# Kernel tuning notes

Measured on AMD Instinct MI355X. Metric: run time of the kernel, lower is better.

## Reference

```python
import jax, jax.numpy as jnp
import numpy as np
import math

B, S, D, H = 2, 2048, 1024, 32
HD = D // H  # head_dim = 32
NEG = -1e9


def setup_inputs() -> dict:
    key = jax.random.key(0)
    ks = jax.random.split(key, 6)
    x = jax.random.normal(ks[0], (B, S, D), dtype=jnp.float32)
    # additive causal mask: 0 on/below diagonal, -1e9 above
    causal = jnp.tril(jnp.ones((S, S), dtype=bool))
    mask = jnp.where(causal, 0.0, NEG).astype(jnp.float32)[None, None]
    # SSMax-style per-query-position log-length scale
    section_log_len = jnp.log(jnp.arange(1, S + 1, dtype=jnp.float32) + 1.0).reshape(1, 1, S, 1)
    sc = 1.0 / math.sqrt(D)
    wq = jax.random.normal(ks[1], (D, D), dtype=jnp.float32) * sc
    wk = jax.random.normal(ks[2], (D, D), dtype=jnp.float32) * sc
    wv = jax.random.normal(ks[3], (D, D), dtype=jnp.float32) * sc
    wo = jax.random.normal(ks[4], (D, D), dtype=jnp.float32) * sc
    seq_scale = jnp.ones((1, H, 1, 1), dtype=jnp.float32)
    return {"x": x, "mask": mask, "section_log_len": section_log_len,
            "wq": wq, "wk": wk, "wv": wv, "wo": wo, "seq_scale": seq_scale}


def reference(x, mask, section_log_len, wq, wk, wv, wo, seq_scale):
    bsz, seqlen, dim = x.shape
    # projections (torch Linear: y = x @ W.T); split heads -> [b, h, s, hd]
    q = (x @ wq.T).reshape(bsz, seqlen, H, HD).transpose(0, 2, 1, 3)
    k = (x @ wk.T).reshape(bsz, seqlen, H, HD).transpose(0, 2, 1, 3)
    v = (x @ wv.T).reshape(bsz, seqlen, H, HD).transpose(0, 2, 1, 3)
    # n_kv_heads == n_heads, so repeat_kv is identity
    scores = jnp.einsum('bhqd,bhkd->bhqk', q, k) / math.sqrt(HD)
    scores = scores * (section_log_len * seq_scale)  # SSMax per-head learned scale
    scores = scores + mask
    probs = jax.nn.softmax(scores.astype(jnp.float32), axis=-1).astype(q.dtype)
    out = jnp.einsum('bhqk,bhkd->bhqd', probs, v)
    out = out.transpose(0, 2, 1, 3).reshape(bsz, seqlen, dim)
    return out @ wo.T
```

## Files before the change

kernel.cpp:

```cpp
#include <hip/hip_runtime.h>
#include <hip/hip_bf16.h>

typedef __bf16 bf16_t;
typedef bf16_t bf16x8 __attribute__((ext_vector_type(8)));
typedef float f32x4 __attribute__((ext_vector_type(4)));

#define NB 2
#define SEQ 2048
#define DIM 1024
#define NH 32
#define HDIM 32

#define LDA 40

static __device__ __forceinline__ f32x4 mfma16(bf16x8 a, bf16x8 b, f32x4 c) {
    return __builtin_amdgcn_mfma_f32_16x16x32_bf16(a, b, c, 0, 0, 0);
}

__global__ __launch_bounds__(256)
void cvt_x(const float* __restrict__ src, bf16_t* __restrict__ dst, int n) {
    const int stride = gridDim.x * blockDim.x;
    const int nv = n >> 2;
    for (int i = blockIdx.x * blockDim.x + threadIdx.x; i < nv; i += stride) {
        float4 v = ((const float4*)src)[i];
        bf16_t o[4] = {(bf16_t)v.x, (bf16_t)v.y, (bf16_t)v.z, (bf16_t)v.w};
        *(uint2*)(dst + i * 4) = *(const uint2*)o;
    }
}

template <int MODE, typename CT>
__global__ __launch_bounds__(256)
void gemm_bt(const bf16_t* __restrict__ A, const float* __restrict__ W,
             CT* __restrict__ C) {
    __shared__ alignas(16) bf16_t As[128 * LDA];
    __shared__ alignas(16) bf16_t Bs[64 * LDA];
    const int t = threadIdx.x;
    const int lane = t & 63;
    const int wave = t >> 6;
    const int lane16 = lane & 15;
    const int quad = lane >> 4;
    const int wm = (wave >> 1) * 64;
    const int wn = (wave & 1) * 32;
    const int m0 = blockIdx.y * 128;
    const int n0 = blockIdx.x * 64;
    const int ar = t >> 2;
    const int ac = (t & 3) * 8;

    f32x4 acc[4][2];
#pragma unroll
    for (int i = 0; i < 4; i++)
#pragma unroll
        for (int j = 0; j < 2; j++) acc[i][j] = f32x4{0.f, 0.f, 0.f, 0.f};

    for (int k0 = 0; k0 < DIM; k0 += 32) {
        uint4 a0 = *(const uint4*)(A + (m0 + ar) * DIM + k0 + ac);
        uint4 a1 = *(const uint4*)(A + (m0 + 64 + ar) * DIM + k0 + ac);
        float4 w0 = *(const float4*)(W + (n0 + ar) * DIM + k0 + ac);
        float4 w1 = *(const float4*)(W + (n0 + ar) * DIM + k0 + ac + 4);
        bf16_t wb[8] = {(bf16_t)w0.x, (bf16_t)w0.y, (bf16_t)w0.z, (bf16_t)w0.w,
                        (bf16_t)w1.x, (bf16_t)w1.y, (bf16_t)w1.z, (bf16_t)w1.w};
        __syncthreads();
        *(uint4*)(As + ar * LDA + ac) = a0;
        *(uint4*)(As + (64 + ar) * LDA + ac) = a1;
        *(uint4*)(Bs + ar * LDA + ac) = *(const uint4*)wb;
        __syncthreads();
        bf16x8 af[4], bfr[2];
#pragma unroll
        for (int mi = 0; mi < 4; mi++)
            af[mi] = *(const bf16x8*)(As + (wm + mi * 16 + lane16) * LDA + quad * 8);
#pragma unroll
        for (int ni = 0; ni < 2; ni++)
            bfr[ni] = *(const bf16x8*)(Bs + (wn + ni * 16 + lane16) * LDA + quad * 8);
#pragma unroll
        for (int mi = 0; mi < 4; mi++)
#pragma unroll
            for (int ni = 0; ni < 2; ni++)
                acc[mi][ni] = (MODE == 2) ? mfma16(bfr[ni], af[mi], acc[mi][ni])
                                          : mfma16(af[mi], bfr[ni], acc[mi][ni]);
    }

#pragma unroll
    for (int mi = 0; mi < 4; mi++)
#pragma unroll
        for (int ni = 0; ni < 2; ni++)
#pragma unroll
            for (int r = 0; r < 4; r++) {
                float v = acc[mi][ni][r];
                if (MODE == 0) {
                    int row = m0 + wm + mi * 16 + quad * 4 + r;
                    int col = n0 + wn + ni * 16 + lane16;
                    C[row * DIM + col] = (CT)v;
                } else if (MODE == 1) {
                    int m = m0 + wm + mi * 16 + quad * 4 + r;
                    int n = n0 + wn + ni * 16 + lane16;
                    int b = m >> 11, s = m & (SEQ - 1);
                    int h = n >> 5, d = n & 31;
                    C[(((b * NH + h) * SEQ + s) << 5) + d] = (CT)v;
                } else {
                    int n = n0 + wn + ni * 16 + quad * 4 + r;
                    int m = m0 + wm + mi * 16 + lane16;
                    int b = m >> 11, s = m & (SEQ - 1);
                    int h = n >> 5, d = n & 31;
                    C[(((b * NH + h) * HDIM + d) << 11) + s] = (CT)v;
                }
            }
}

__global__ __launch_bounds__(256)
void attn_fwd(const bf16_t* __restrict__ q, const bf16_t* __restrict__ k,
              const bf16_t* __restrict__ vt, const float* __restrict__ slen,
              const float* __restrict__ sscale, bf16_t* __restrict__ out) {
    __shared__ alignas(16) bf16_t pscr[4][32 * LDA];
    const int t = threadIdx.x;
    const int lane = t & 63, wave = t >> 6;
    const int lane16 = lane & 15, quad = lane >> 4;
    const int gw = blockIdx.x * 4 + wave;
    const int idx = gw & 63;
    const int qt = (idx & 1) ? (63 - (idx >> 1)) : (idx >> 1);
    const int h = (gw >> 6) & (NH - 1);
    const int b = gw >> 11;
    const int q0 = qt * 32;
    const bf16_t* qh = q + (b * NH + h) * SEQ * HDIM;
    const bf16_t* kh = k + (b * NH + h) * SEQ * HDIM;
    const bf16_t* vth = vt + (b * NH + h) * HDIM * SEQ;
    bf16_t* psw = pscr[wave];

    bf16x8 qf[2];
    qf[0] = *(const bf16x8*)(qh + (q0 + lane16) * HDIM + quad * 8);
    qf[1] = *(const bf16x8*)(qh + (q0 + 16 + lane16) * HDIM + quad * 8);

    const float hs = sscale[h] * 0.17677669529663687f;
    float rs[2][4];
#pragma unroll
    for (int mi = 0; mi < 2; mi++)
#pragma unroll
        for (int r = 0; r < 4; r++)
            rs[mi][r] = slen[q0 + mi * 16 + quad * 4 + r] * hs;

    f32x4 o[2][2];
    float lrow[2][4];
#pragma unroll
    for (int mi = 0; mi < 2; mi++)
#pragma unroll
        for (int r = 0; r < 4; r++) lrow[mi][r] = 0.f;
#pragma unroll
    for (int mi = 0; mi < 2; mi++)
#pragma unroll
        for (int ni = 0; ni < 2; ni++) o[mi][ni] = f32x4{0.f, 0.f, 0.f, 0.f};

    const bf16_t* kp0 = kh + (2 * lane16) * HDIM + quad * 8;
    const bf16_t* vp0 = vth + lane16 * SEQ + quad * 8;
    const bf16_t* vp1 = vth + (16 + lane16) * SEQ + quad * 8;

    auto process = [&](bf16x8 kf0, bf16x8 kf1, int kv, bool domask) {
        const f32x4 zz = f32x4{0.f, 0.f, 0.f, 0.f};
        f32x4 sc[2][2];
        sc[0][0] = mfma16(qf[0], kf0, zz);
        sc[0][1] = mfma16(qf[0], kf1, zz);
        sc[1][0] = mfma16(qf[1], kf0, zz);
        sc[1][1] = mfma16(qf[1], kf1, zz);
        bf16x8 vf0 = *(const bf16x8*)(vp0 + kv);
        bf16x8 vf1 = *(const bf16x8*)(vp1 + kv);
#pragma unroll
        for (int mi = 0; mi < 2; mi++)
#pragma unroll
            for (int r = 0; r < 4; r++) {
                float p0 = __expf(sc[mi][0][r] * rs[mi][r]);
                float p1 = __expf(sc[mi][1][r] * rs[mi][r]);
                if (domask) {
                    const int rowloc = mi * 16 + quad * 4 + r;
                    if (2 * lane16 > rowloc) p0 = 0.f;
                    if (2 * lane16 + 1 > rowloc) p1 = 0.f;
                }
                lrow[mi][r] += p0 + p1;
                bf16_t pb[2] = {(bf16_t)p0, (bf16_t)p1};
                *(unsigned int*)(psw + (mi * 16 + quad * 4 + r) * LDA +
                                 2 * lane16) = *(const unsigned int*)pb;
            }
        asm volatile("s_waitcnt lgkmcnt(0)" ::: "memory");
        bf16x8 pf0 = *(const bf16x8*)(psw + lane16 * LDA + quad * 8);
        bf16x8 pf1 = *(const bf16x8*)(psw + (16 + lane16) * LDA + quad * 8);
        o[0][0] = mfma16(pf0, vf0, o[0][0]);
        o[0][1] = mfma16(pf0, vf1, o[0][1]);
        o[1][0] = mfma16(pf1, vf0, o[1][0]);
        o[1][1] = mfma16(pf1, vf1, o[1][1]);
    };

    bf16x8 kc0 = *(const bf16x8*)(kp0);
    bf16x8 kc1 = *(const bf16x8*)(kp0 + HDIM);
    for (int kv = 0; kv < q0; kv += 32) {
        bf16x8 kn0 = *(const bf16x8*)(kp0 + (kv + 32) * HDIM);
        bf16x8 kn1 = *(const bf16x8*)(kp0 + (kv + 32) * HDIM + HDIM);
        process(kc0, kc1, kv, false);
        kc0 = kn0;
        kc1 = kn1;
    }
    process(kc0, kc1, q0, true);

#pragma unroll
    for (int mi = 0; mi < 2; mi++)
#pragma unroll
        for (int r = 0; r < 4; r++) {
            float l = lrow[mi][r];
#pragma unroll
            for (int off = 1; off < 16; off <<= 1) l += __shfl_xor(l, off);
            float inv = 1.0f / l;
            int qi = q0 + mi * 16 + quad * 4 + r;
            float* dummy;
            (void)dummy;
            bf16_t* ob = out + (b * SEQ + qi) * DIM + h * HDIM;
#pragma unroll
            for (int ni = 0; ni < 2; ni++)
                ob[ni * 16 + lane16] = (bf16_t)(o[mi][ni][r] * inv);
        }
}

extern "C" void kernel_launch(void* const* d_in, const int* in_sizes, int n_in,
                              void* d_out, int out_size, void* d_ws, size_t ws_size,
                              hipStream_t stream) {
    const float* x = (const float*)d_in[0];
    const float* slen = (const float*)d_in[2];
    const float* wq = (const float*)d_in[3];
    const float* wk = (const float*)d_in[4];
    const float* wv = (const float*)d_in[5];
    const float* wo = (const float*)d_in[6];
    const float* ss = (const float*)d_in[7];

    const size_t ELEMS = (size_t)NB * SEQ * DIM;
    bf16_t* xb = (bf16_t*)d_ws;
    bf16_t* abuf = xb;
    bf16_t* qbuf = xb + ELEMS;
    bf16_t* vtbuf = qbuf + ELEMS;
    bf16_t* kbuf = (bf16_t*)d_out;

    dim3 blk(256);
    cvt_x<<<dim3(512), blk, 0, stream>>>(x, xb, (int)ELEMS);

    dim3 grd(DIM / 64, (NB * SEQ) / 128);
    gemm_bt<1, bf16_t><<<grd, blk, 0, stream>>>(xb, wq, qbuf);
    gemm_bt<1, bf16_t><<<grd, blk, 0, stream>>>(xb, wk, kbuf);
    gemm_bt<2, bf16_t><<<grd, blk, 0, stream>>>(xb, wv, vtbuf);
    attn_fwd<<<dim3(NB * NH * (SEQ / 32) / 4), blk, 0, stream>>>(
        qbuf, kbuf, vtbuf, slen, ss, abuf);
    gemm_bt<0, float><<<grd, blk, 0, stream>>>(abuf, wo, (float*)d_out);
}
```

Measured before the change: 254.0 us.

## Fuse QKV projections into one GEMM with LDS-direct loads and pre-converted weights

The weights are converted to bf16 in a single batched conversion kernel, so the GEMM no longer converts fp32 inside its main loop. The three Q/K/V projection launches become one launch over a concatenated weight matrix, with a 128x128 tile and a per-block epilogue that routes each tile to the Q, K or transposed V layout. Tiles are loaded through global_load_lds straight into unpadded LDS. The attention softmax also switches to exp2 with log2(e) folded into the scale. The unpadded LDS layout may cause bank conflicts, and each call pays for a conversion pass over all weights.

```diff
diff --git a/kernel.cpp b/kernel.cpp
--- a/kernel.cpp
+++ b/kernel.cpp
@@ -17,93 +17,132 @@
     return __builtin_amdgcn_mfma_f32_16x16x32_bf16(a, b, c, 0, 0, 0);
 }
 
+static __device__ __forceinline__ void load_lds16(const bf16_t* g, bf16_t* l) {
+    __builtin_amdgcn_global_load_lds(
+        (const __attribute__((address_space(1))) void*)(g),
+        (__attribute__((address_space(3))) void*)(l), 16, 0, 0);
+}
+
 __global__ __launch_bounds__(256)
-void cvt_x(const float* __restrict__ src, bf16_t* __restrict__ dst, int n) {
+void cvt_f32_bf16(const float* __restrict__ s0, bf16_t* __restrict__ d0, int n0,
+                  const float* __restrict__ s1, bf16_t* __restrict__ d1, int n1,
+                  const float* __restrict__ s2, bf16_t* __restrict__ d2, int n2,
+                  const float* __restrict__ s3, bf16_t* __restrict__ d3, int n3,
+                  const float* __restrict__ s4, bf16_t* __restrict__ d4, int n4) {
     const int stride = gridDim.x * blockDim.x;
-    const int nv = n >> 2;
-    for (int i = blockIdx.x * blockDim.x + threadIdx.x; i < nv; i += stride) {
-        float4 v = ((const float4*)src)[i];
-        bf16_t o[4] = {(bf16_t)v.x, (bf16_t)v.y, (bf16_t)v.z, (bf16_t)v.w};
-        *(uint2*)(dst + i * 4) = *(const uint2*)o;
-    }
-}
-
-template <int MODE, typename CT>
+    const int tid = blockIdx.x * blockDim.x + threadIdx.x;
+    const float* src[5] = {s0, s1, s2, s3, s4};
+    bf16_t* dst[5] = {d0, d1, d2, d3, d4};
+    const int n[5] = {n0, n1, n2, n3, n4};
+#pragma unroll
+    for (int r = 0; r < 5; r++) {
+        const int nv = n[r] >> 2;
+        for (int i = tid; i < nv; i += stride) {
+            float4 v = ((const float4*)src[r])[i];
+            bf16_t o[4] = {(bf16_t)v.x, (bf16_t)v.y, (bf16_t)v.z, (bf16_t)v.w};
+            *(uint2*)(dst[r] + i * 4) = *(const uint2*)o;
+        }
+    }
+}
+
+template <int EPI>
 __global__ __launch_bounds__(256)
-void gemm_bt(const bf16_t* __restrict__ A, const float* __restrict__ W,
-             CT* __restrict__ C) {
-    __shared__ alignas(16) bf16_t As[128 * LDA];
-    __shared__ alignas(16) bf16_t Bs[64 * LDA];
+void gemm128(const bf16_t* __restrict__ A, const bf16_t* __restrict__ W,
+             float* __restrict__ Cf, bf16_t* __restrict__ qb,
+             bf16_t* __restrict__ kb, bf16_t* __restrict__ vtb) {
+    __shared__ alignas(16) bf16_t As[128 * 32];
+    __shared__ alignas(16) bf16_t Bs[128 * 32];
     const int t = threadIdx.x;
-    const int lane = t & 63;
-    const int wave = t >> 6;
-    const int lane16 = lane & 15;
-    const int quad = lane >> 4;
-    const int wm = (wave >> 1) * 64;
-    const int wn = (wave & 1) * 32;
+    const int lane = t & 63, wave = t >> 6;
+    const int lane16 = lane & 15, quad = lane >> 4;
+    const int wm = (wave >> 1) * 64, wn = (wave & 1) * 64;
     const int m0 = blockIdx.y * 128;
-    const int n0 = blockIdx.x * 64;
-    const int ar = t >> 2;
-    const int ac = (t & 3) * 8;
-
-    f32x4 acc[4][2];
+    const int n0g = blockIdx.x * 128;
+    const int tr = t >> 2;
+    const int tc = (t & 3) * 8;
+    bf16_t* ldsA = As + (t & 192) * 8;
+    bf16_t* ldsB = Bs + (t & 192) * 8;
+    const bf16_t* ga = A + (m0 + tr) * DIM + tc;
+    const bf16_t* gb = W + (n0g + tr) * DIM + tc;
+
+    const bool vseg = (EPI == 1) && (n0g >= 2048);
+
+    f32x4 acc[4][4];
 #pragma unroll
     for (int i = 0; i < 4; i++)
 #pragma unroll
-        for (int j = 0; j < 2; j++) acc[i][j] = f32x4{0.f, 0.f, 0.f, 0.f};
+        for (int j = 0; j < 4; j++) acc[i][j] = f32x4{0.f, 0.f, 0.f, 0.f};
 
     for (int k0 = 0; k0 < DIM; k0 += 32) {
-        uint4 a0 = *(const uint4*)(A + (m0 + ar) * DIM + k0 + ac);
-        uint4 a1 = *(const uint4*)(A + (m0 + 64 + ar) * DIM + k0 + ac);
-        float4 w0 = *(const float4*)(W + (n0 + ar) * DIM + k0 + ac);
-        float4 w1 = *(const float4*)(W + (n0 + ar) * DIM + k0 + ac + 4);
-        bf16_t wb[8] = {(bf16_t)w0.x, (bf16_t)w0.y, (bf16_t)w0.z, (bf16_t)w0.w,
-                        (bf16_t)w1.x, (bf16_t)w1.y, (bf16_t)w1.z, (bf16_t)w1.w};
         __syncthreads();
-        *(uint4*)(As + ar * LDA + ac) = a0;
-        *(uint4*)(As + (64 + ar) * LDA + ac) = a1;
-        *(uint4*)(Bs + ar * LDA + ac) = *(const uint4*)wb;
+        load_lds16(ga + k0, ldsA);
+        load_lds16(ga + 64 * DIM + k0, ldsA + 64 * 32);
+        load_lds16(gb + k0, ldsB);
+        load_lds16(gb + 64 * DIM + k0, ldsB + 64 * 32);
         __syncthreads();
-        bf16x8 af[4], bfr[2];
-#pragma unroll
-        for (int mi = 0; mi < 4; mi++)
-            af[mi] = *(const bf16x8*)(As + (wm + mi * 16 + lane16) * LDA + quad * 8);
-#pragma unroll
-        for (int ni = 0; ni < 2; ni++)
-            bfr[ni] = *(const bf16x8*)(Bs + (wn + ni * 16 + lane16) * LDA + quad * 8);
-#pragma unroll
-        for (int mi = 0; mi < 4; mi++)
-#pragma unroll
-            for (int ni = 0; ni < 2; ni++)
-                acc[mi][ni] = (MODE == 2) ? mfma16(bfr[ni], af[mi], acc[mi][ni])
-                                          : mfma16(af[mi], bfr[ni], acc[mi][ni]);
-    }
-
-#pragma unroll
-    for (int mi = 0; mi < 4; mi++)
-#pragma unroll
-        for (int ni = 0; ni < 2; ni++)
-#pragma unroll
-            for (int r = 0; r < 4; r++) {
-                float v = acc[mi][ni][r];
-                if (MODE == 0) {
+        bf16x8 af[4], bfr[4];
+#pragma unroll
+        for (int mi = 0; mi < 4; mi++)
+            af[mi] = *(const bf16x8*)(As + (wm + mi * 16 + lane16) * 32 + quad * 8);
+#pragma unroll
+        for (int ni = 0; ni < 4; ni++)
+            bfr[ni] = *(const bf16x8*)(Bs + (wn + ni * 16 + lane16) * 32 + quad * 8);
+        if (vseg) {
+#pragma unroll
+            for (int mi = 0; mi < 4; mi++)
+#pragma unroll
+                for (int ni = 0; ni < 4; ni++)
+                    acc[mi][ni] = mfma16(bfr[ni], af[mi], acc[mi][ni]);
+        } else {
+#pragma unroll
+            for (int mi = 0; mi < 4; mi++)
+#pragma unroll
+                for (int ni = 0; ni < 4; ni++)
+                    acc[mi][ni] = mfma16(af[mi], bfr[ni], acc[mi][ni]);
+        }
+    }
+
+    if (EPI == 0) {
+#pragma unroll
+        for (int mi = 0; mi < 4; mi++)
+#pragma unroll
+            for (int ni = 0; ni < 4; ni++)
+#pragma unroll
+                for (int r = 0; r < 4; r++) {
                     int row = m0 + wm + mi * 16 + quad * 4 + r;
-                    int col = n0 + wn + ni * 16 + lane16;
-                    C[row * DIM + col] = (CT)v;
-                } else if (MODE == 1) {
+                    int col = n0g + wn + ni * 16 + lane16;
+                    Cf[row * DIM + col] = acc[mi][ni][r];
+                }
+    } else if (!vseg) {
+        bf16_t* dst = (n0g < 1024) ? qb : kb;
+        const int nb = n0g & 1023;
+#pragma unroll
+        for (int mi = 0; mi < 4; mi++)
+#pragma unroll
+            for (int ni = 0; ni < 4; ni++)
+#pragma unroll
+                for (int r = 0; r < 4; r++) {
                     int m = m0 + wm + mi * 16 + quad * 4 + r;
-                    int n = n0 + wn + ni * 16 + lane16;
+                    int nl = nb + wn + ni * 16 + lane16;
                     int b = m >> 11, s = m & (SEQ - 1);
-                    int h = n >> 5, d = n & 31;
-                    C[(((b * NH + h) * SEQ + s) << 5) + d] = (CT)v;
-                } else {
-                    int n = n0 + wn + ni * 16 + quad * 4 + r;
+                    int h = nl >> 5, d = nl & 31;
+                    dst[(((b * NH + h) << 11) + s) * 32 + d] = (bf16_t)acc[mi][ni][r];
+                }
+    } else {
+        const int nb = n0g & 1023;
+#pragma unroll
+        for (int mi = 0; mi < 4; mi++)
+#pragma unroll
+            for (int ni = 0; ni < 4; ni++)
+#pragma unroll
+                for (int r = 0; r < 4; r++) {
+                    int nl = nb + wn + ni * 16 + quad * 4 + r;
                     int m = m0 + wm + mi * 16 + lane16;
                     int b = m >> 11, s = m & (SEQ - 1);
-                    int h = n >> 5, d = n & 31;
-                    C[(((b * NH + h) * HDIM + d) << 11) + s] = (CT)v;
-                }
-            }
+                    int h = nl >> 5, d = nl & 31;
+                    vtb[(((b * NH + h) << 5) + d) * SEQ + s] = (bf16_t)acc[mi][ni][r];
+                }
+    }
 }
 
 __global__ __launch_bounds__(256)
@@ -129,7 +168,7 @@
     qf[0] = *(const bf16x8*)(qh + (q0 + lane16) * HDIM + quad * 8);
     qf[1] = *(const bf16x8*)(qh + (q0 + 16 + lane16) * HDIM + quad * 8);
 
-    const float hs = sscale[h] * 0.17677669529663687f;
+    const float hs = sscale[h] * 0.17677669529663687f * 1.4426950408889634f;
     float rs[2][4];
 #pragma unroll
     for (int mi = 0; mi < 2; mi++)
@@ -165,8 +204,8 @@
         for (int mi = 0; mi < 2; mi++)
 #pragma unroll
             for (int r = 0; r < 4; r++) {
-                float p0 = __expf(sc[mi][0][r] * rs[mi][r]);
-                float p1 = __expf(sc[mi][1][r] * rs[mi][r]);
+                float p0 = exp2f(sc[mi][0][r] * rs[mi][r]);
+                float p1 = exp2f(sc[mi][1][r] * rs[mi][r]);
                 if (domask) {
                     const int rowloc = mi * 16 + quad * 4 + r;
                     if (2 * lane16 > rowloc) p0 = 0.f;
@@ -206,8 +245,6 @@
             for (int off = 1; off < 16; off <<= 1) l += __shfl_xor(l, off);
             float inv = 1.0f / l;
             int qi = q0 + mi * 16 + quad * 4 + r;
-            float* dummy;
-            (void)dummy;
             bf16_t* ob = out + (b * SEQ + qi) * DIM + h * HDIM;
 #pragma unroll
             for (int ni = 0; ni < 2; ni++)
@@ -227,20 +264,24 @@
     const float* ss = (const float*)d_in[7];
 
     const size_t ELEMS = (size_t)NB * SEQ * DIM;
+    const size_t WELEMS = (size_t)DIM * DIM;
     bf16_t* xb = (bf16_t*)d_ws;
     bf16_t* abuf = xb;
-    bf16_t* qbuf = xb + ELEMS;
+    bf16_t* wqkvb = xb + ELEMS;
+    bf16_t* wob = wqkvb + 3 * WELEMS;
+    bf16_t* qbuf = wob + WELEMS;
     bf16_t* vtbuf = qbuf + ELEMS;
     bf16_t* kbuf = (bf16_t*)d_out;
 
     dim3 blk(256);
-    cvt_x<<<dim3(512), blk, 0, stream>>>(x, xb, (int)ELEMS);
-
-    dim3 grd(DIM / 64, (NB * SEQ) / 128);
-    gemm_bt<1, bf16_t><<<grd, blk, 0, stream>>>(xb, wq, qbuf);
-    gemm_bt<1, bf16_t><<<grd, blk, 0, stream>>>(xb, wk, kbuf);
-    gemm_bt<2, bf16_t><<<grd, blk, 0, stream>>>(xb, wv, vtbuf);
+    cvt_f32_bf16<<<dim3(1024), blk, 0, stream>>>(
+        x, xb, (int)ELEMS, wq, wqkvb, (int)WELEMS, wk, wqkvb + WELEMS,
+        (int)WELEMS, wv, wqkvb + 2 * WELEMS, (int)WELEMS, wo, wob, (int)WELEMS);
+
+    gemm128<1><<<dim3(3 * DIM / 128, (NB * SEQ) / 128), blk, 0, stream>>>(
+        xb, wqkvb, nullptr, qbuf, kbuf, vtbuf);
     attn_fwd<<<dim3(NB * NH * (SEQ / 32) / 4), blk, 0, stream>>>(
         qbuf, kbuf, vtbuf, slen, ss, abuf);
-    gemm_bt<0, float><<<grd, blk, 0, stream>>>(abuf, wo, (float*)d_out);
-}
+    gemm128<0><<<dim3(DIM / 128, (NB * SEQ) / 128), blk, 0, stream>>>(
+        abuf, wob, (float*)d_out, nullptr, nullptr, nullptr);
+}
```

New measurement: 235.0 us. 1.08x faster.
